# Kernel tuning notes

Hardware: AMD Instinct MI355X
Metric: run time of the kernel (lower is better)

## Reference

```python
import jax, jax.numpy as jnp
import numpy as np

NUM_NODES = 256
IN_FEAT = 64
HIDDEN = 512
N_CLASSES = 2
BATCH = 256


def setup_inputs() -> dict:
    key = jax.random.key(0)
    ks = jax.random.split(key, 10)
    return {
        "z": jax.random.normal(ks[0], (BATCH, 1, NUM_NODES, NUM_NODES), dtype=jnp.float32),
        "node_emb": jax.random.normal(ks[1], (NUM_NODES, IN_FEAT), dtype=jnp.float32),
        "w1": jax.random.normal(ks[2], (IN_FEAT, HIDDEN), dtype=jnp.float32) * (1.0 / np.sqrt(IN_FEAT)),
        "b1": jnp.zeros((HIDDEN,), dtype=jnp.float32),
        "w2": jax.random.normal(ks[3], (HIDDEN, HIDDEN), dtype=jnp.float32) * (1.0 / np.sqrt(HIDDEN)),
        "b2": jnp.zeros((HIDDEN,), dtype=jnp.float32),
        "w3": jax.random.normal(ks[4], (HIDDEN, HIDDEN), dtype=jnp.float32) * (1.0 / np.sqrt(HIDDEN)),
        "b3": jnp.zeros((HIDDEN,), dtype=jnp.float32),
        "fcw": jax.random.normal(ks[5], (HIDDEN, N_CLASSES), dtype=jnp.float32) * (1.0 / np.sqrt(HIDDEN)),
        "fcb": jnp.zeros((N_CLASSES,), dtype=jnp.float32),
    }


def reference(z, node_emb, w1, b1, w2, b2, w3, b3, fcw, fcb):
    # z: (B, 1, N, N) latent interpreted as weighted adjacency
    z_sq = jnp.squeeze(z, axis=1)                         # (B, N, N)
    A = jax.nn.sigmoid(z_sq)
    A = (A + jnp.swapaxes(A, 1, 2)) * 0.5                  # symmetrize
    A_hat = A + jnp.eye(A.shape[-1], dtype=A.dtype)[None]  # add self loops
    D_hat = jnp.sum(A_hat, axis=2) + 1e-6                  # (B, N) degrees
    d_inv_sqrt = D_hat ** -0.5
    # norm_A = D^{-1/2} A_hat D^{-1/2} via row/col scaling (same math as diag bmm)
    norm_A = A_hat * d_inv_sqrt[:, :, None] * d_inv_sqrt[:, None, :]

    X = jnp.broadcast_to(node_emb[None], (z.shape[0],) + node_emb.shape)  # (B, N, F)
    H1 = jax.nn.relu(jnp.einsum('bij,bjh->bih', norm_A, X @ w1 + b1))
    H2 = jax.nn.relu(jnp.einsum('bij,bjh->bih', norm_A, H1 @ w2 + b2))
    H3 = jax.nn.relu(jnp.einsum('bij,bjh->bih', norm_A, H2 @ w3 + b3))
    graph_emb = jnp.mean(H3, axis=1)                       # (B, H)
    logits = graph_emb @ fcw + fcb                         # (B, n_classes)
    return logits
```

## Files before the change

### kernel.cpp

```cpp
#include <hip/hip_runtime.h>
#include <stdint.h>

#define B_ 256
#define N_ 256
#define F_ 64
#define H_ 512

typedef _Float16 f16;
typedef _Float16 f16x8 __attribute__((ext_vector_type(8)));
typedef _Float16 f16x4 __attribute__((ext_vector_type(4)));
typedef float    f32x4 __attribute__((ext_vector_type(4)));

__device__ __forceinline__ float sigmoidf_(float x) {
    return 1.0f / (1.0f + __expf(-x));
}

__global__ __launch_bounds__(256) void k_sums(const float* __restrict__ z,
                                              f16* __restrict__ S,
                                              float* __restrict__ R,
                                              float* __restrict__ Cg) {
    int b = blockIdx.y, c = blockIdx.x;
    int tid = threadIdx.x, lane = tid & 63, w = tid >> 6;
    float colacc[4] = {0.f, 0.f, 0.f, 0.f};
    for (int r = 0; r < 16; r++) {
        int i = c * 64 + w * 16 + r;
        size_t base = ((size_t)(b * N_ + i)) * N_;
        float4 v = *(const float4*)(z + base + lane * 4);
        float s0 = sigmoidf_(v.x), s1 = sigmoidf_(v.y),
              s2 = sigmoidf_(v.z), s3 = sigmoidf_(v.w);
        f16x4 sv = { (f16)s0, (f16)s1, (f16)s2, (f16)s3 };
        *(f16x4*)(S + base + lane * 4) = sv;
        colacc[0] += s0; colacc[1] += s1; colacc[2] += s2; colacc[3] += s3;
        float rs = s0 + s1 + s2 + s3;
        for (int off = 32; off; off >>= 1) rs += __shfl_down(rs, off, 64);
        if (lane == 0) R[b * N_ + i] = rs;
    }
    __shared__ float cbuf[4][N_];
    #pragma unroll
    for (int k = 0; k < 4; k++) cbuf[w][lane * 4 + k] = colacc[k];
    __syncthreads();
    float s = cbuf[0][tid] + cbuf[1][tid] + cbuf[2][tid] + cbuf[3][tid];
    atomicAdd(Cg + b * N_ + tid, s);
}

__global__ __launch_bounds__(256) void k_norma3(const f16* __restrict__ S,
                                                const float* __restrict__ R,
                                                const float* __restrict__ Cg,
                                                f16* __restrict__ nA) {
    __shared__ f16 T0[128 * 129];
    __shared__ f16 T1[128 * 129];
    __shared__ float Dv[N_];
    int b = blockIdx.y, t = blockIdx.x;
    int tid = threadIdx.x;
    const f16* Sb = S + (size_t)b * N_ * N_;
    f16* Ab = nA + (size_t)b * N_ * N_;

    Dv[tid] = rsqrtf(1.0f + 1e-6f + 0.5f * (R[b * N_ + tid] + Cg[b * N_ + tid]));

    auto stage = [&](const f16* src, f16* dst) {
        #pragma unroll
        for (int it = 0; it < 8; it++) {
            int u = it * 256 + tid;
            int r = u >> 4, c8 = (u & 15) * 8;
            *(f16x8*)&dst[r * 129 + c8] = *(const f16x8*)&src[(size_t)r * N_ + c8];
        }
    };
    if (t == 0)      stage(Sb, T0);
    else if (t == 1) stage(Sb + 128 * N_ + 128, T0);
    else           { stage(Sb + 128, T0); stage(Sb + (size_t)128 * N_, T1); }
    __syncthreads();

    auto emit = [&](const f16* Dir, const f16* Mir, int i0, int j0) {
        #pragma unroll
        for (int it = 0; it < 8; it++) {
            int il = it * 16 + (tid >> 4), jl8 = (tid & 15) * 8;
            float di = Dv[i0 + il];
            f16x8 d = *(const f16x8*)&Dir[il * 129 + jl8];
            f16x8 o;
            #pragma unroll
            for (int k = 0; k < 8; k++) {
                float v = 0.5f * ((float)d[k] + (float)Mir[(jl8 + k) * 129 + il]);
                if (i0 + il == j0 + jl8 + k) v += 1.0f;
                o[k] = (f16)(v * di * Dv[j0 + jl8 + k]);
            }
            *(f16x8*)&Ab[(size_t)(i0 + il) * N_ + j0 + jl8] = o;
        }
    };
    if (t == 0)      emit(T0, T0, 0, 0);
    else if (t == 1) emit(T0, T0, 128, 128);
    else           { emit(T0, T1, 0, 128); emit(T1, T0, 128, 0); }
}

__global__ __launch_bounds__(256) void k_xw1(const float* __restrict__ ne,
                                             const float* __restrict__ w1,
                                             const float* __restrict__ b1,
                                             f16* __restrict__ XW1t) {
    int h = blockIdx.x;
    int node = threadIdx.x;
    float s = b1[h];
    #pragma unroll 8
    for (int k = 0; k < F_; k++) s += ne[node * F_ + k] * w1[k * H_ + h];
    XW1t[h * N_ + node] = (f16)s;
}

__global__ __launch_bounds__(256) void k_wt(const float* __restrict__ w2,
                                            const float* __restrict__ w3,
                                            f16* __restrict__ w2t,
                                            f16* __restrict__ w3t) {
    int which = blockIdx.y;
    const float* src = which ? w3 : w2;
    f16* dst = which ? w3t : w2t;
    int idx = blockIdx.x * 256 + threadIdx.x;
    int k = idx >> 9, n = idx & 511;
    dst[n * H_ + k] = (f16)src[k * H_ + n];
}

template <int KDIM, int MODE>
__global__ __launch_bounds__(256) void k_gemm(const f16* __restrict__ A, long aBatch,
                                              const f16* __restrict__ Bt, long bBatch,
                                              f16* __restrict__ Out,
                                              const float* __restrict__ bias,
                                              float* __restrict__ g) {
    __shared__ f16 As[128 * 64];
    __shared__ f16 Bs[128 * 64];
    const int tid  = threadIdx.x;
    const int lane = tid & 63, wave = tid >> 6;
    const int wm = wave >> 1, wn = wave & 1;

    const int lin = blockIdx.x;
    const int xcd = lin & 7, q = lin >> 3;
    const int n_t = q & 3, p = q >> 2;
    const int gp  = xcd * 64 + p;
    const int b   = gp >> 1, m_t = gp & 1;
    const int m0 = m_t * 128, n0 = n_t * 128;

    const f16* Ab = A + (size_t)b * aBatch;
    const f16* Bb = Bt + (size_t)b * bBatch;

    f32x4 acc[4][4];
    #pragma unroll
    for (int i = 0; i < 4; i++)
        #pragma unroll
        for (int j = 0; j < 4; j++)
            #pragma unroll
            for (int r = 0; r < 4; r++) acc[i][j][r] = 0.0f;

    const int lr = lane >> 3;
    const int kc = (lane & 7) ^ lr;

    for (int kk = 0; kk < KDIM; kk += 64) {
        #pragma unroll
        for (int c = 0; c < 4; c++) {
            int chunk = wave * 4 + c;
            int row = chunk * 8 + lr;
            __builtin_amdgcn_global_load_lds(
                (__attribute__((address_space(1))) void*)(Ab + (size_t)(m0 + row) * KDIM + kk + kc * 8),
                (__attribute__((address_space(3))) void*)(&As[chunk * 512]), 16, 0, 0);
            __builtin_amdgcn_global_load_lds(
                (__attribute__((address_space(1))) void*)(Bb + (size_t)(n0 + row) * KDIM + kk + kc * 8),
                (__attribute__((address_space(3))) void*)(&Bs[chunk * 512]), 16, 0, 0);
        }
        __syncthreads();

        #pragma unroll
        for (int ks = 0; ks < 2; ks++) {
            f16x8 aF[4], bF[4];
            #pragma unroll
            for (int t = 0; t < 4; t++) {
                int rowA = wm * 64 + t * 16 + (lane & 15);
                int rowB = wn * 64 + t * 16 + (lane & 15);
                int rkc  = ks * 4 + (lane >> 4);
                aF[t] = *(const f16x8*)&As[(rowA * 8 + (rkc ^ (rowA & 7))) * 8];
                bF[t] = *(const f16x8*)&Bs[(rowB * 8 + (rkc ^ (rowB & 7))) * 8];
            }
            #pragma unroll
            for (int mt = 0; mt < 4; mt++)
                #pragma unroll
                for (int nt = 0; nt < 4; nt++)
                    acc[mt][nt] = __builtin_amdgcn_mfma_f32_16x16x32_f16(aF[mt], bF[nt], acc[mt][nt], 0, 0, 0);
        }
        __syncthreads();
    }

    const int quad = lane >> 4, ln15 = lane & 15;
    if (MODE == 0) {
        f16* Ob = Out + (size_t)b * (N_ * H_);
        #pragma unroll
        for (int mt = 0; mt < 4; mt++) {
            int node = m0 + wm * 64 + mt * 16 + quad * 4;
            #pragma unroll
            for (int nt = 0; nt < 4; nt++) {
                int h = n0 + wn * 64 + nt * 16 + ln15;
                #pragma unroll
                for (int rr = 0; rr < 4; rr++) {
                    float v = acc[mt][nt][rr];
                    v = v > 0.f ? v : 0.f;
                    Ob[(size_t)(node + rr) * H_ + h] = (f16)v;
                }
            }
        }
    } else if (MODE == 1) {
        f16* Ob = Out + (size_t)b * (H_ * N_);
        #pragma unroll
        for (int nt = 0; nt < 4; nt++) {
            int n = n0 + wn * 64 + nt * 16 + ln15;
            float bv = bias[n];
            #pragma unroll
            for (int mt = 0; mt < 4; mt++) {
                int node = m0 + wm * 64 + mt * 16 + quad * 4;
                f16x4 v;
                #pragma unroll
                for (int rr = 0; rr < 4; rr++) v[rr] = (f16)(acc[mt][nt][rr] + bv);
                *(f16x4*)&Ob[(size_t)n * N_ + node] = v;
            }
        }
    } else {
        #pragma unroll
        for (int nt = 0; nt < 4; nt++) {
            float partial = 0.f;
            #pragma unroll
            for (int mt = 0; mt < 4; mt++)
                #pragma unroll
                for (int rr = 0; rr < 4; rr++) {
                    float v = acc[mt][nt][rr];
                    partial += (v > 0.f ? v : 0.f);
                }
            partial += __shfl_down(partial, 32, 64);
            partial += __shfl_down(partial, 16, 64);
            if (quad == 0) {
                int h = n0 + wn * 64 + nt * 16 + ln15;
                atomicAdd(g + b * H_ + h, partial);
            }
        }
    }
}

__global__ __launch_bounds__(256) void k_logits(const float* __restrict__ g,
                                                const float* __restrict__ fcw,
                                                const float* __restrict__ fcb,
                                                float* __restrict__ out) {
    int b = blockIdx.x, tid = threadIdx.x;
    const float* gb = g + b * H_;
    float g0 = gb[tid], g1 = gb[tid + 256];
    float p0 = g0 * fcw[tid * 2 + 0] + g1 * fcw[(tid + 256) * 2 + 0];
    float p1 = g0 * fcw[tid * 2 + 1] + g1 * fcw[(tid + 256) * 2 + 1];
    for (int off = 32; off; off >>= 1) {
        p0 += __shfl_down(p0, off, 64);
        p1 += __shfl_down(p1, off, 64);
    }
    __shared__ float r0[4], r1[4];
    int lane = tid & 63, w = tid >> 6;
    if (lane == 0) { r0[w] = p0; r1[w] = p1; }
    __syncthreads();
    const float inv = 1.0f / N_;
    if (tid == 0) out[b * 2 + 0] = (r0[0] + r0[1] + r0[2] + r0[3]) * inv + fcb[0];
    if (tid == 1) out[b * 2 + 1] = (r1[0] + r1[1] + r1[2] + r1[3]) * inv + fcb[1];
}

extern "C" void kernel_launch(void* const* d_in, const int* in_sizes, int n_in,
                              void* d_out, int out_size, void* d_ws, size_t ws_size,
                              hipStream_t stream) {
    const float* z   = (const float*)d_in[0];
    const float* ne  = (const float*)d_in[1];
    const float* w1  = (const float*)d_in[2];
    const float* b1  = (const float*)d_in[3];
    const float* w2  = (const float*)d_in[4];
    const float* b2  = (const float*)d_in[5];
    const float* w3  = (const float*)d_in[6];
    const float* b3  = (const float*)d_in[7];
    const float* fcw = (const float*)d_in[8];
    const float* fcb = (const float*)d_in[9];
    float* out = (float*)d_out;

    char* ws = (char*)d_ws;
    f16*   T    = (f16*)(ws + 0);
    float* R    = (float*)(ws + 0);
    float* Cg   = (float*)(ws + 262144);
    f16*   nA   = (f16*)(ws + 67108864);
    f16*   Hh   = (f16*)(ws + 100663296);
    f16*   S    = (f16*)(ws + 100663296);
    float* g    = (float*)(ws + 100663296);
    f16*   XW1t = (f16*)(ws + 167772160);
    f16*   w2t  = (f16*)(ws + 168034304);
    f16*   w3t  = (f16*)(ws + 168558592);

    hipMemsetAsync(Cg, 0, N_ * B_ * sizeof(float), stream);
    k_sums  <<<dim3(4, B_), 256, 0, stream>>>(z, S, R, Cg);
    k_norma3<<<dim3(3, B_), 256, 0, stream>>>(S, R, Cg, nA);
    k_xw1<<<H_,            256, 0, stream>>>(ne, w1, b1, XW1t);
    k_wt <<<dim3(1024, 2), 256, 0, stream>>>(w2, w3, w2t, w3t);

    k_gemm<256, 0><<<2048, 256, 0, stream>>>(nA, 65536, XW1t, 0, Hh, nullptr, nullptr);
    k_gemm<512, 1><<<2048, 256, 0, stream>>>(Hh, 131072, w2t, 0, T, b2, nullptr);
    k_gemm<256, 0><<<2048, 256, 0, stream>>>(nA, 65536, T, 131072, Hh, nullptr, nullptr);
    k_gemm<512, 1><<<2048, 256, 0, stream>>>(Hh, 131072, w3t, 0, T, b3, nullptr);
    hipMemsetAsync(g, 0, B_ * H_ * sizeof(float), stream);
    k_gemm<256, 2><<<2048, 256, 0, stream>>>(nA, 65536, T, 131072, Hh, nullptr, g);

    k_logits<<<B_, 256, 0, stream>>>(g, fcw, fcb, out);
}
```

Before: 346.4 us.

## Double-buffer GEMM LDS tiles and replace atomics/memsets with partial-sum buffers

The GEMM now keeps two LDS stages and issues the global-to-LDS loads for the next K slice before computing on the current one. This lets load latency overlap with MFMA work and removes one barrier per iteration. The column-sum and graph-embedding reductions now write per-block partial buffers instead of using atomicAdd, and the consumers sum those partials, so both hipMemsetAsync calls go away. The cost is twice the LDS per block, which may lower occupancy, plus a small extra partial-buffer read in the consumers.

```diff
diff --git a/kernel.cpp b/kernel.cpp
--- a/kernel.cpp
+++ b/kernel.cpp
@@ -18,7 +18,7 @@
 __global__ __launch_bounds__(256) void k_sums(const float* __restrict__ z,
                                               f16* __restrict__ S,
                                               float* __restrict__ R,
-                                              float* __restrict__ Cg) {
+                                              float* __restrict__ Cpart) {
     int b = blockIdx.y, c = blockIdx.x;
     int tid = threadIdx.x, lane = tid & 63, w = tid >> 6;
     float colacc[4] = {0.f, 0.f, 0.f, 0.f};
@@ -39,13 +39,13 @@
     #pragma unroll
     for (int k = 0; k < 4; k++) cbuf[w][lane * 4 + k] = colacc[k];
     __syncthreads();
-    float s = cbuf[0][tid] + cbuf[1][tid] + cbuf[2][tid] + cbuf[3][tid];
-    atomicAdd(Cg + b * N_ + tid, s);
+    float s4 = cbuf[0][tid] + cbuf[1][tid] + cbuf[2][tid] + cbuf[3][tid];
+    Cpart[((size_t)c * B_ + b) * N_ + tid] = s4;
 }
 
 __global__ __launch_bounds__(256) void k_norma3(const f16* __restrict__ S,
                                                 const float* __restrict__ R,
-                                                const float* __restrict__ Cg,
+                                                const float* __restrict__ Cpart,
                                                 f16* __restrict__ nA) {
     __shared__ f16 T0[128 * 129];
     __shared__ f16 T1[128 * 129];
@@ -55,7 +55,11 @@
     const f16* Sb = S + (size_t)b * N_ * N_;
     f16* Ab = nA + (size_t)b * N_ * N_;
 
-    Dv[tid] = rsqrtf(1.0f + 1e-6f + 0.5f * (R[b * N_ + tid] + Cg[b * N_ + tid]));
+    float cs = Cpart[(size_t)b * N_ + tid]
+             + Cpart[((size_t)B_ + b) * N_ + tid]
+             + Cpart[((size_t)2 * B_ + b) * N_ + tid]
+             + Cpart[((size_t)3 * B_ + b) * N_ + tid];
+    Dv[tid] = rsqrtf(1.0f + 1e-6f + 0.5f * (R[b * N_ + tid] + cs));
 
     auto stage = [&](const f16* src, f16* dst) {
         #pragma unroll
@@ -120,9 +124,9 @@
                                               const f16* __restrict__ Bt, long bBatch,
                                               f16* __restrict__ Out,
                                               const float* __restrict__ bias,
-                                              float* __restrict__ g) {
-    __shared__ f16 As[128 * 64];
-    __shared__ f16 Bs[128 * 64];
+                                              float* __restrict__ gp) {
+    __shared__ f16 As[2][128 * 64];
+    __shared__ f16 Bs[2][128 * 64];
     const int tid  = threadIdx.x;
     const int lane = tid & 63, wave = tid >> 6;
     const int wm = wave >> 1, wn = wave & 1;
@@ -130,8 +134,8 @@
     const int lin = blockIdx.x;
     const int xcd = lin & 7, q = lin >> 3;
     const int n_t = q & 3, p = q >> 2;
-    const int gp  = xcd * 64 + p;
-    const int b   = gp >> 1, m_t = gp & 1;
+    const int grp = xcd * 64 + p;
+    const int b   = grp >> 1, m_t = grp & 1;
     const int m0 = m_t * 128, n0 = n_t * 128;
 
     const f16* Ab = A + (size_t)b * aBatch;
@@ -148,20 +152,29 @@
     const int lr = lane >> 3;
     const int kc = (lane & 7) ^ lr;
 
-    for (int kk = 0; kk < KDIM; kk += 64) {
+    auto issue = [&](int kk, int buf) {
         #pragma unroll
         for (int c = 0; c < 4; c++) {
             int chunk = wave * 4 + c;
             int row = chunk * 8 + lr;
             __builtin_amdgcn_global_load_lds(
                 (__attribute__((address_space(1))) void*)(Ab + (size_t)(m0 + row) * KDIM + kk + kc * 8),
-                (__attribute__((address_space(3))) void*)(&As[chunk * 512]), 16, 0, 0);
+                (__attribute__((address_space(3))) void*)(&As[buf][chunk * 512]), 16, 0, 0);
             __builtin_amdgcn_global_load_lds(
                 (__attribute__((address_space(1))) void*)(Bb + (size_t)(n0 + row) * KDIM + kk + kc * 8),
-                (__attribute__((address_space(3))) void*)(&Bs[chunk * 512]), 16, 0, 0);
-        }
-        __syncthreads();
-
+                (__attribute__((address_space(3))) void*)(&Bs[buf][chunk * 512]), 16, 0, 0);
+        }
+    };
+
+    issue(0, 0);
+    __syncthreads();
+
+    constexpr int NS = KDIM / 64;
+    #pragma unroll
+    for (int s = 0; s < NS; s++) {
+        if (s + 1 < NS) issue((s + 1) * 64, (s + 1) & 1);
+        const f16* Ac = As[s & 1];
+        const f16* Bc = Bs[s & 1];
         #pragma unroll
         for (int ks = 0; ks < 2; ks++) {
             f16x8 aF[4], bF[4];
@@ -170,8 +183,8 @@
                 int rowA = wm * 64 + t * 16 + (lane & 15);
                 int rowB = wn * 64 + t * 16 + (lane & 15);
                 int rkc  = ks * 4 + (lane >> 4);
-                aF[t] = *(const f16x8*)&As[(rowA * 8 + (rkc ^ (rowA & 7))) * 8];
-                bF[t] = *(const f16x8*)&Bs[(rowB * 8 + (rkc ^ (rowB & 7))) * 8];
+                aF[t] = *(const f16x8*)&Ac[(rowA * 8 + (rkc ^ (rowA & 7))) * 8];
+                bF[t] = *(const f16x8*)&Bc[(rowB * 8 + (rkc ^ (rowB & 7))) * 8];
             }
             #pragma unroll
             for (int mt = 0; mt < 4; mt++)
@@ -179,7 +192,7 @@
                 for (int nt = 0; nt < 4; nt++)
                     acc[mt][nt] = __builtin_amdgcn_mfma_f32_16x16x32_f16(aF[mt], bF[nt], acc[mt][nt], 0, 0, 0);
         }
-        __syncthreads();
+        if (s + 1 < NS) __syncthreads();
     }
 
     const int quad = lane >> 4, ln15 = lane & 15;
@@ -215,6 +228,7 @@
             }
         }
     } else {
+        float part[4];
         #pragma unroll
         for (int nt = 0; nt < 4; nt++) {
             float partial = 0.f;
@@ -227,21 +241,33 @@
                 }
             partial += __shfl_down(partial, 32, 64);
             partial += __shfl_down(partial, 16, 64);
-            if (quad == 0) {
-                int h = n0 + wn * 64 + nt * 16 + ln15;
-                atomicAdd(g + b * H_ + h, partial);
-            }
+            part[nt] = partial;
+        }
+        __syncthreads();
+        float* red = (float*)&As[0][0];
+        if (quad == 0) {
+            #pragma unroll
+            for (int nt = 0; nt < 4; nt++)
+                red[wave * 64 + nt * 16 + ln15] = part[nt];
+        }
+        __syncthreads();
+        if (tid < 128) {
+            int wnl = tid >> 6, hl = tid & 63;
+            float v = red[wnl * 64 + hl] + red[(wnl + 2) * 64 + hl];
+            gp[((size_t)m_t * B_ + b) * H_ + n0 + wnl * 64 + hl] = v;
         }
     }
 }
 
-__global__ __launch_bounds__(256) void k_logits(const float* __restrict__ g,
+__global__ __launch_bounds__(256) void k_logits(const float* __restrict__ gp,
                                                 const float* __restrict__ fcw,
                                                 const float* __restrict__ fcb,
                                                 float* __restrict__ out) {
     int b = blockIdx.x, tid = threadIdx.x;
-    const float* gb = g + b * H_;
-    float g0 = gb[tid], g1 = gb[tid + 256];
+    const float* g0p = gp + (size_t)b * H_;
+    const float* g1p = gp + (size_t)(B_ + b) * H_;
+    float g0 = g0p[tid] + g1p[tid];
+    float g1 = g0p[tid + 256] + g1p[tid + 256];
     float p0 = g0 * fcw[tid * 2 + 0] + g1 * fcw[(tid + 256) * 2 + 0];
     float p1 = g0 * fcw[tid * 2 + 1] + g1 * fcw[(tid + 256) * 2 + 1];
     for (int off = 32; off; off >>= 1) {
@@ -273,20 +299,19 @@
     float* out = (float*)d_out;
 
     char* ws = (char*)d_ws;
-    f16*   T    = (f16*)(ws + 0);
-    float* R    = (float*)(ws + 0);
-    float* Cg   = (float*)(ws + 262144);
-    f16*   nA   = (f16*)(ws + 67108864);
-    f16*   Hh   = (f16*)(ws + 100663296);
-    f16*   S    = (f16*)(ws + 100663296);
-    float* g    = (float*)(ws + 100663296);
-    f16*   XW1t = (f16*)(ws + 167772160);
-    f16*   w2t  = (f16*)(ws + 168034304);
-    f16*   w3t  = (f16*)(ws + 168558592);
-
-    hipMemsetAsync(Cg, 0, N_ * B_ * sizeof(float), stream);
-    k_sums  <<<dim3(4, B_), 256, 0, stream>>>(z, S, R, Cg);
-    k_norma3<<<dim3(3, B_), 256, 0, stream>>>(S, R, Cg, nA);
+    f16*   T     = (f16*)(ws + 0);
+    float* R     = (float*)(ws + 0);
+    float* Cpart = (float*)(ws + 262144);
+    f16*   nA    = (f16*)(ws + 67108864);
+    f16*   Hh    = (f16*)(ws + 100663296);
+    f16*   S     = (f16*)(ws + 100663296);
+    float* gpart = (float*)(ws + 100663296);
+    f16*   XW1t  = (f16*)(ws + 167772160);
+    f16*   w2t   = (f16*)(ws + 168034304);
+    f16*   w3t   = (f16*)(ws + 168558592);
+
+    k_sums  <<<dim3(4, B_), 256, 0, stream>>>(z, S, R, Cpart);
+    k_norma3<<<dim3(3, B_), 256, 0, stream>>>(S, R, Cpart, nA);
     k_xw1<<<H_,            256, 0, stream>>>(ne, w1, b1, XW1t);
     k_wt <<<dim3(1024, 2), 256, 0, stream>>>(w2, w3, w2t, w3t);
 
@@ -294,8 +319,7 @@
     k_gemm<512, 1><<<2048, 256, 0, stream>>>(Hh, 131072, w2t, 0, T, b2, nullptr);
     k_gemm<256, 0><<<2048, 256, 0, stream>>>(nA, 65536, T, 131072, Hh, nullptr, nullptr);
     k_gemm<512, 1><<<2048, 256, 0, stream>>>(Hh, 131072, w3t, 0, T, b3, nullptr);
-    hipMemsetAsync(g, 0, B_ * H_ * sizeof(float), stream);
-    k_gemm<256, 2><<<2048, 256, 0, stream>>>(nA, 65536, T, 131072, Hh, nullptr, g);
-
-    k_logits<<<B_, 256, 0, stream>>>(g, fcw, fcb, out);
-}
+    k_gemm<256, 2><<<2048, 256, 0, stream>>>(nA, 65536, T, 131072, nullptr, nullptr, gpart);
+
+    k_logits<<<B_, 256, 0, stream>>>(gpart, fcw, fcb, out);
+}
```

Result: slower. 402.3 us (+16.1%).
